# Kernel optimization log

Hardware: AMD Instinct MI355X
Metric: run time of the kernel (lower is better)

## Reference

```python
import jax, jax.numpy as jnp
import numpy as np

B, N, DIM = 4, 2048, 1024
HEADS, DHEAD = 16, 64
INNER = HEADS * DHEAD  # 1024


def _sigma(t):
    # elu(x) + 1 feature map (strictly positive)
    return jax.nn.elu(t) + 1.0


def setup_inputs() -> dict:
    key = jax.random.key(0)
    k1, k2, k3, k4, k5 = jax.random.split(key, 5)
    x = jax.random.normal(k1, (B, N, DIM), dtype=jnp.float32)
    M = jax.random.normal(k2, (B, HEADS, DHEAD, DHEAD), dtype=jnp.float32)
    Z = jnp.ones((B, HEADS, DHEAD, 1), dtype=jnp.float32)
    W_qkv = jax.random.normal(k3, (DIM, 3 * INNER), dtype=jnp.float32) * (DIM ** -0.5)
    beta_lin = jnp.ones((1,), dtype=jnp.float32) * 4.6     # Linear_Attention.beta
    beta_gate = jax.random.normal(k4, (1, HEADS, 1, 1), dtype=jnp.float32)  # per-head gate
    return {"x": x, "M": M, "Z": Z, "W_qkv": W_qkv, "beta_lin": beta_lin, "beta_gate": beta_gate}


def reference(x, M, Z, W_qkv, beta_lin, beta_gate):
    b, n, _ = x.shape
    scale = DHEAD ** -0.5

    qkv = x @ W_qkv                                   # [b, n, 3*inner]
    q, k, v = jnp.split(qkv, 3, axis=-1)
    # b n (h d) -> b h n d
    to_heads = lambda t: t.reshape(b, n, HEADS, DHEAD).transpose(0, 2, 1, 3)
    q, k, v = to_heads(q), to_heads(k), to_heads(v)

    # ---- linear-attention compressive memory branch ----
    sq = _sigma(q)                                    # [b h n d]
    sk = _sigma(k)
    A_mem = jnp.einsum('bhnd,bhdv->bhnv', sq, M) / jnp.einsum('bhnd,bhdi->bhni', sq, Z)
    moment = jnp.einsum('bhnd,bhdv->bhnv', sk, M) / jnp.einsum('bhnd,bhdi->bhni', sk, Z)

    # EMA state update (training path)
    beta_m = jnp.clip(jax.nn.sigmoid(beta_lin), 0.9, 0.999)  # scalar in (0.9, 0.999)
    Z_new = beta_m * Z + jnp.sum(sk, axis=-2)[..., None]      # [b h d 1]
    M_new = beta_m * M + jnp.einsum('bhnd,bhnv->bhdv', sk, v - moment)

    # ---- standard dot-product attention branch ----
    dots = jnp.einsum('bhid,bhjd->bhij', q, k) * scale
    attn = jax.nn.softmax(dots, axis=-1)
    A_dot = jnp.einsum('bhij,bhjd->bhid', attn, v)

    # ---- learned per-head gate ----
    g = jax.nn.sigmoid(beta_gate)                     # [1 h 1 1]
    A = g * A_mem + (1.0 - g) * A_dot                 # [b h n d]
    A = A.transpose(0, 2, 1, 3).reshape(b, n, INNER)  # b h n d -> b n (h d)
    return (A, M_new, Z_new)
```

## Files before the change

kernel.cpp:

```cpp
#include <hip/hip_runtime.h>
#include <math.h>

#define B_ 4
#define N_ 2048
#define DIM_ 1024
#define H_ 16
#define D_ 64
#define INNER_ 1024
#define BH_ (B_*H_)

#define A_ELEMS  (B_*N_*INNER_)
#define M_ELEMS  (BH_*D_*D_)
#define Z_ELEMS  (BH_*D_)

typedef __attribute__((ext_vector_type(8))) short short8;
typedef __attribute__((ext_vector_type(4))) float f32x4;
typedef __attribute__((ext_vector_type(4))) unsigned short us4;
typedef unsigned short u16;

__device__ __forceinline__ u16 f2bf(float f) {
    unsigned int u = __float_as_uint(f);
    u += 0x7fffu + ((u >> 16) & 1u);
    return (u16)(u >> 16);
}
__device__ __forceinline__ float bf2f(u16 s) {
    return __uint_as_float(((unsigned int)s) << 16);
}
__device__ __forceinline__ float sigma_f(float x) {
    return x > 0.f ? x + 1.f : __expf(x);
}
__device__ __forceinline__ short8 sig8(short8 in) {
    short8 out;
    u16* ip = (u16*)&in; u16* op = (u16*)&out;
    #pragma unroll
    for (int c = 0; c < 8; c++) op[c] = f2bf(sigma_f(bf2f(ip[c])));
    return out;
}

__global__ __launch_bounds__(256) void cvt_x(const float* __restrict__ x,
                                             u16* __restrict__ xb) {
    long i = ((long)blockIdx.x * 256 + threadIdx.x) * 4;
    float4 f = *(const float4*)&x[i];
    us4 o = {f2bf(f.x), f2bf(f.y), f2bf(f.z), f2bf(f.w)};
    *(us4*)&xb[i] = o;
}

__global__ __launch_bounds__(256) void cvt_w(const float* __restrict__ W,
                                             u16* __restrict__ Wt) {
    __shared__ u16 T[64 * 68];
    const int t  = threadIdx.x;
    const int n0 = blockIdx.x * 64, k0 = blockIdx.y * 64;
    #pragma unroll
    for (int i = 0; i < 4; i++) {
        int r  = (t >> 4) + i * 16;
        int c4 = (t & 15) * 4;
        float4 f = *(const float4*)&W[(long)(k0 + r) * 3072 + n0 + c4];
        T[(c4 + 0) * 68 + r] = f2bf(f.x);
        T[(c4 + 1) * 68 + r] = f2bf(f.y);
        T[(c4 + 2) * 68 + r] = f2bf(f.z);
        T[(c4 + 3) * 68 + r] = f2bf(f.w);
    }
    __syncthreads();
    #pragma unroll
    for (int i = 0; i < 4; i++) {
        int n  = (t >> 4) + i * 16;
        int k4 = (t & 15) * 4;
        us4 o;
        o.x = T[n * 68 + k4];     o.y = T[n * 68 + k4 + 1];
        o.z = T[n * 68 + k4 + 2]; o.w = T[n * 68 + k4 + 3];
        *(us4*)&Wt[(long)(n0 + n) * 1024 + k0 + k4] = o;
    }
}

__global__ __launch_bounds__(256) void qkv_mfma(
    const u16* __restrict__ xb, const u16* __restrict__ Wt,
    u16* __restrict__ q, u16* __restrict__ k, u16* __restrict__ v) {
    __shared__ u16 As[128 * 40];
    __shared__ u16 Bs[128 * 40];
    const int t = threadIdx.x, w = t >> 6, lane = t & 63;
    const int quad = lane >> 4, l16 = lane & 15;
    const int m0 = blockIdx.y * 128, j0 = blockIdx.x * 128;
    const int mw = (w >> 1) * 64, nw = (w & 1) * 64;

    f32x4 acc[4][4] = {};

    for (int k0 = 0; k0 < DIM_; k0 += 32) {
        __syncthreads();
        #pragma unroll
        for (int i = 0; i < 2; i++) {
            int r = (t >> 2) + i * 64, kg = (t & 3) * 8;
            *(short8*)&As[r * 40 + kg] =
                *(const short8*)&xb[(long)(m0 + r) * 1024 + k0 + kg];
            *(short8*)&Bs[r * 40 + kg] =
                *(const short8*)&Wt[(long)(j0 + r) * 1024 + k0 + kg];
        }
        __syncthreads();

        short8 af[4], bf[4];
        #pragma unroll
        for (int mt = 0; mt < 4; mt++)
            af[mt] = *(const short8*)&As[(mw + mt * 16 + l16) * 40 + quad * 8];
        #pragma unroll
        for (int nt = 0; nt < 4; nt++)
            bf[nt] = *(const short8*)&Bs[(nw + nt * 16 + l16) * 40 + quad * 8];
        #pragma unroll
        for (int mt = 0; mt < 4; mt++)
            #pragma unroll
            for (int nt = 0; nt < 4; nt++)
                acc[mt][nt] = __builtin_amdgcn_mfma_f32_16x16x32_bf16(
                    af[mt], bf[nt], acc[mt][nt], 0, 0, 0);
    }

    #pragma unroll
    for (int mt = 0; mt < 4; mt++) {
        #pragma unroll
        for (int r = 0; r < 4; r++) {
            int mm = m0 + mw + mt * 16 + quad * 4 + r;
            int b  = mm >> 11, n = mm & 2047;
            #pragma unroll
            for (int nt = 0; nt < 4; nt++) {
                int col   = j0 + nw + nt * 16 + l16;
                int which = col >> 10;
                int rem   = col & 1023;
                int h = rem >> 6, d = rem & 63;
                u16* dst = (which == 0) ? q : (which == 1) ? k : v;
                dst[(((long)(b * H_ + h)) * N_ + n) * D_ + d] =
                    f2bf(acc[mt][nt][r]);
            }
        }
    }
}

__global__ __launch_bounds__(256) void init_mz(
    const float* __restrict__ M, const float* __restrict__ Z,
    const float* __restrict__ beta_lin,
    float* __restrict__ outM, float* __restrict__ outZ) {
    float beta = 1.f / (1.f + __expf(-beta_lin[0]));
    beta = fminf(fmaxf(beta, 0.9f), 0.999f);
    int i = blockIdx.x * 256 + threadIdx.x;
    if (i < M_ELEMS) outM[i] = beta * M[i];
    if (i < Z_ELEMS) outZ[i] = beta * Z[i];
}

__global__ __launch_bounds__(256) void linear_mfma(
    const u16* __restrict__ qg, const u16* __restrict__ kg_,
    const u16* __restrict__ vg, const float* __restrict__ Mg,
    const float* __restrict__ Zg, const float* __restrict__ beta_gate,
    float* __restrict__ outA, float* __restrict__ outM, float* __restrict__ outZ) {
    __shared__ u16 MTz[80 * 72];
    __shared__ u16 sqsh[64 * 72];
    __shared__ u16 sksh[64 * 72];
    __shared__ u16 skT[64 * 72];
    __shared__ u16 vT[64 * 72];
    __shared__ u16 vmT[80 * 72];
    __shared__ float dks[64];

    const int bh = blockIdx.y, b = bh >> 4, h = bh & 15;
    const int t = threadIdx.x, w = t >> 6, lane = t & 63;
    const int quad = lane >> 4, l16 = lane & 15;
    const long bhN = (long)bh * N_;

    #pragma unroll
    for (int i = 0; i < 4; i++) {
        int d  = (t >> 4) + i * 16;
        int c4 = (t & 15) * 4;
        float4 f = *(const float4*)&Mg[bh * 4096 + d * 64 + c4];
        MTz[(c4 + 0) * 72 + d] = f2bf(f.x);
        MTz[(c4 + 1) * 72 + d] = f2bf(f.y);
        MTz[(c4 + 2) * 72 + d] = f2bf(f.z);
        MTz[(c4 + 3) * 72 + d] = f2bf(f.w);
    }
    if (t < 64) {
        MTz[64 * 72 + t] = f2bf(Zg[bh * 64 + t]);
        vmT[64 * 72 + t] = f2bf(1.0f);
    }
    for (int e = t; e < 15 * 72; e += 256) {
        MTz[65 * 72 + e] = 0;
        vmT[65 * 72 + e] = 0;
    }
    if (t >= 64 && t < 72) { MTz[64 * 72 + t] = 0; vmT[64 * 72 + t] = 0; }

    const float g = 1.f / (1.f + __expf(-beta_gate[h]));

    f32x4 macc[5] = {};

    const int jj = t >> 3;
    const int kgp = (t & 7) * 8;

    for (int c0 = 0; c0 < 256; c0 += 64) {
        const int n0c = blockIdx.x * 256 + c0;
        __syncthreads();

        #pragma unroll
        for (int i = 0; i < 2; i++) {
            int j = jj + i * 32;
            long gb = ((bhN + n0c + j) << 6) + kgp;
            short8 q8 = sig8(*(const short8*)&qg[gb]);
            short8 k8 = sig8(*(const short8*)&kg_[gb]);
            short8 v8 = *(const short8*)&vg[gb];
            *(short8*)&sqsh[j * 72 + kgp] = q8;
            *(short8*)&sksh[j * 72 + kgp] = k8;
            u16* kp = (u16*)&k8;
            u16* vp = (u16*)&v8;
            int jc = j ^ kgp;
            #pragma unroll
            for (int c = 0; c < 8; c++) {
                skT[(kgp + c) * 72 + jc] = kp[c];
                vT[(kgp + c) * 72 + jc]  = vp[c];
            }
        }
        __syncthreads();

        {
            short8 a0 = *(const short8*)&sqsh[(w * 16 + l16) * 72 + quad * 8];
            short8 a1 = *(const short8*)&sqsh[(w * 16 + l16) * 72 + 32 + quad * 8];
            f32x4 am[5];
            #pragma unroll
            for (int ct = 0; ct < 5; ct++) {
                short8 b0 = *(const short8*)&MTz[(ct * 16 + l16) * 72 + quad * 8];
                short8 b1 = *(const short8*)&MTz[(ct * 16 + l16) * 72 + 32 + quad * 8];
                f32x4 acc = {};
                acc = __builtin_amdgcn_mfma_f32_16x16x32_bf16(a0, b0, acc, 0, 0, 0);
                acc = __builtin_amdgcn_mfma_f32_16x16x32_bf16(a1, b1, acc, 0, 0, 0);
                am[ct] = acc;
            }
            #pragma unroll
            for (int r = 0; r < 4; r++) {
                float dq  = __shfl(am[4][r], lane & 48, 64);
                float inv = __builtin_amdgcn_rcpf(dq);
                int n = n0c + w * 16 + quad * 4 + r;
                long row = ((long)(b * N_ + n)) * INNER_ + h * 64;
                #pragma unroll
                for (int ct = 0; ct < 4; ct++)
                    outA[row + ct * 16 + l16] = g * am[ct][r] * inv;
            }
        }

        f32x4 mt_[4];
        {
            short8 a0 = *(const short8*)&MTz[(w * 16 + l16) * 72 + quad * 8];
            short8 a1 = *(const short8*)&MTz[(w * 16 + l16) * 72 + 32 + quad * 8];
            #pragma unroll
            for (int ct = 0; ct < 4; ct++) {
                short8 b0 = *(const short8*)&sksh[(ct * 16 + l16) * 72 + quad * 8];
                short8 b1 = *(const short8*)&sksh[(ct * 16 + l16) * 72 + 32 + quad * 8];
                f32x4 acc = {};
                acc = __builtin_amdgcn_mfma_f32_16x16x32_bf16(a0, b0, acc, 0, 0, 0);
                acc = __builtin_amdgcn_mfma_f32_16x16x32_bf16(a1, b1, acc, 0, 0, 0);
                mt_[ct] = acc;
            }
            short8 z0 = *(const short8*)&MTz[(64 + l16) * 72 + quad * 8];
            short8 z1 = *(const short8*)&MTz[(64 + l16) * 72 + 32 + quad * 8];
            short8 b0 = *(const short8*)&sksh[(w * 16 + l16) * 72 + quad * 8];
            short8 b1 = *(const short8*)&sksh[(w * 16 + l16) * 72 + 32 + quad * 8];
            f32x4 acc = {};
            acc = __builtin_amdgcn_mfma_f32_16x16x32_bf16(z0, b0, acc, 0, 0, 0);
            acc = __builtin_amdgcn_mfma_f32_16x16x32_bf16(z1, b1, acc, 0, 0, 0);
            if (quad == 0) dks[w * 16 + l16] = __builtin_amdgcn_rcpf(acc[0]);
        }
        __syncthreads();

        #pragma unroll
        for (int ct = 0; ct < 4; ct++) {
            float invdk = dks[ct * 16 + l16];
            #pragma unroll
            for (int r = 0; r < 4; r++) {
                int vd = w * 16 + quad * 4 + r;
                float vv = bf2f(vT[vd * 72 + ((ct * 16 + l16) ^ (vd & 56))]);
                vmT[vd * 72 + ct * 16 + l16] = f2bf(vv - mt_[ct][r] * invdk);
            }
        }
        __syncthreads();

        {
            int drow = w * 16 + l16, xr = drow & 56;
            short8 a0 = *(const short8*)&skT[drow * 72 + ((quad * 8) ^ xr)];
            short8 a1 = *(const short8*)&skT[drow * 72 + ((32 + quad * 8) ^ xr)];
            #pragma unroll
            for (int ct = 0; ct < 5; ct++) {
                short8 b0 = *(const short8*)&vmT[(ct * 16 + l16) * 72 + quad * 8];
                short8 b1 = *(const short8*)&vmT[(ct * 16 + l16) * 72 + 32 + quad * 8];
                macc[ct] = __builtin_amdgcn_mfma_f32_16x16x32_bf16(a0, b0, macc[ct], 0, 0, 0);
                macc[ct] = __builtin_amdgcn_mfma_f32_16x16x32_bf16(a1, b1, macc[ct], 0, 0, 0);
            }
        }
    }

    #pragma unroll
    for (int ct = 0; ct < 4; ct++)
        #pragma unroll
        for (int r = 0; r < 4; r++) {
            int d = w * 16 + quad * 4 + r;
            atomicAdd(&outM[bh * 4096 + d * 64 + ct * 16 + l16], macc[ct][r]);
        }
    if (l16 == 0)
        #pragma unroll
        for (int r = 0; r < 4; r++)
            atomicAdd(&outZ[bh * 64 + w * 16 + quad * 4 + r], macc[4][r]);
}

__global__ __launch_bounds__(256) void flash_mfma(
    const u16* __restrict__ qb, const u16* __restrict__ kb,
    const u16* __restrict__ vb, const float* __restrict__ beta_gate,
    float* __restrict__ outA) {
    __shared__ u16 Ks[64 * 72];
    __shared__ u16 Vt[64 * 72];
    __shared__ u16 Ps[4][32 * 72];

    const int bh = blockIdx.y, b = bh >> 4, h = bh & 15;
    const int n0 = blockIdx.x * 128;
    const int t = threadIdx.x, w = t >> 6, lane = t & 63;
    const int quad = lane >> 4, l16 = lane & 15;
    const long bhN = (long)bh * N_;

    short8 qf[2][2];
    #pragma unroll
    for (int mi = 0; mi < 2; mi++) {
        long qrow = bhN + n0 + w * 32 + mi * 16 + l16;
        qf[mi][0] = *(const short8*)&qb[(qrow << 6) + quad * 8];
        qf[mi][1] = *(const short8*)&qb[(qrow << 6) + 32 + quad * 8];
    }

    f32x4 of[2][4] = {};
    float lpart[2] = {0.f, 0.f};

    for (int j0 = 0; j0 < N_; j0 += 64) {
        __syncthreads();
        #pragma unroll
        for (int i = 0; i < 2; i++) {
            int j  = (t >> 3) + i * 32;
            int kg = (t & 7) * 8;
            long gbase = ((bhN + j0 + j) << 6) + kg;
            *(short8*)&Ks[j * 72 + kg] = *(const short8*)&kb[gbase];
            short8 vv = *(const short8*)&vb[gbase];
            u16* vp = (u16*)&vv;
            int jc = j ^ kg;
            #pragma unroll
            for (int c = 0; c < 8; c++) Vt[(kg + c) * 72 + jc] = vp[c];
        }
        __syncthreads();

        #pragma unroll
        for (int kt = 0; kt < 4; kt++) {
            short8 kf0 = *(const short8*)&Ks[(kt * 16 + l16) * 72 + quad * 8];
            short8 kf1 = *(const short8*)&Ks[(kt * 16 + l16) * 72 + 32 + quad * 8];
            #pragma unroll
            for (int mi = 0; mi < 2; mi++) {
                f32x4 st = {};
                st = __builtin_amdgcn_mfma_f32_16x16x32_bf16(kf0, qf[mi][0], st, 0, 0, 0);
                st = __builtin_amdgcn_mfma_f32_16x16x32_bf16(kf1, qf[mi][1], st, 0, 0, 0);
                float p0 = __expf(st[0] * 0.125f);
                float p1 = __expf(st[1] * 0.125f);
                float p2 = __expf(st[2] * 0.125f);
                float p3 = __expf(st[3] * 0.125f);
                lpart[mi] += (p0 + p1) + (p2 + p3);
                uint2 pk;
                pk.x = (__float_as_uint(p0) >> 16) | (__float_as_uint(p1) & 0xFFFF0000u);
                pk.y = (__float_as_uint(p2) >> 16) | (__float_as_uint(p3) & 0xFFFF0000u);
                *(uint2*)&Ps[w][(mi * 16 + l16) * 72 + kt * 16 + quad * 4] = pk;
            }
        }

        #pragma unroll
        for (int s = 0; s < 2; s++) {
            short8 af0 = *(const short8*)&Ps[w][(l16) * 72 + s * 32 + quad * 8];
            short8 af1 = *(const short8*)&Ps[w][(16 + l16) * 72 + s * 32 + quad * 8];
            #pragma unroll
            for (int nt = 0; nt < 4; nt++) {
                int d  = nt * 16 + l16;
                int xr = d & 56;
                short8 vf = *(const short8*)&Vt[d * 72 + ((s * 32 + quad * 8) ^ xr)];
                of[0][nt] = __builtin_amdgcn_mfma_f32_16x16x32_bf16(af0, vf, of[0][nt], 0, 0, 0);
                of[1][nt] = __builtin_amdgcn_mfma_f32_16x16x32_bf16(af1, vf, of[1][nt], 0, 0, 0);
            }
        }
    }

    const float g  = 1.f / (1.f + __expf(-beta_gate[h]));
    const float gi = 1.f - g;
    #pragma unroll
    for (int mi = 0; mi < 2; mi++) {
        float lr = lpart[mi];
        lr += __shfl_xor(lr, 16, 64);
        lr += __shfl_xor(lr, 32, 64);
        float linv = 1.f / lr;
        #pragma unroll
        for (int r = 0; r < 4; r++) {
            float lv = __shfl(linv, quad * 4 + r, 64);
            int n = n0 + w * 32 + mi * 16 + quad * 4 + r;
            #pragma unroll
            for (int nt = 0; nt < 4; nt++) {
                long idx = ((long)(b * N_ + n)) * INNER_ + h * 64 + nt * 16 + l16;
                outA[idx] += gi * of[mi][nt][r] * lv;
            }
        }
    }
}

extern "C" void kernel_launch(void* const* d_in, const int* in_sizes, int n_in,
                              void* d_out, int out_size, void* d_ws, size_t ws_size,
                              hipStream_t stream) {
    const float* x         = (const float*)d_in[0];
    const float* M         = (const float*)d_in[1];
    const float* Z         = (const float*)d_in[2];
    const float* W         = (const float*)d_in[3];
    const float* beta_lin  = (const float*)d_in[4];
    const float* beta_gate = (const float*)d_in[5];

    float* out  = (float*)d_out;
    float* outA = out;
    float* outM = out + A_ELEMS;
    float* outZ = out + A_ELEMS + M_ELEMS;

    u16* xb = (u16*)d_ws;
    u16* Wt = xb + (size_t)8192 * 1024;
    u16* qb = Wt + (size_t)3072 * 1024;
    u16* kb = qb + (size_t)BH_ * N_ * D_;
    u16* vb = kb + (size_t)BH_ * N_ * D_;

    cvt_x<<<dim3(A_ELEMS / 1024), 256, 0, stream>>>(x, xb);
    cvt_w<<<dim3(48, 16), 256, 0, stream>>>(W, Wt);
    qkv_mfma<<<dim3(24, 64), 256, 0, stream>>>(xb, Wt, qb, kb, vb);
    init_mz<<<dim3((M_ELEMS + 255) / 256), 256, 0, stream>>>(M, Z, beta_lin, outM, outZ);
    linear_mfma<<<dim3(8, BH_), 256, 0, stream>>>(qb, kb, vb, M, Z, beta_gate,
                                                  outA, outM, outZ);
    flash_mfma<<<dim3(N_ / 128, BH_), 256, 0, stream>>>(qb, kb, vb, beta_gate, outA);
}
```

Before: 309.5 us.

## Store V pre-transposed from QKV GEMM and register-prefetch K/V tiles in flash kernel

The QKV GEMM epilogue now writes V in a [bh, d, n] transposed layout, so the linear and flash kernels can stage V into shared memory with vector stores instead of scalar transposing scatters. The flash kernel also prefetches the next K/V tile into registers while the current tile is being computed. It additionally replaces expf with exp2 using a prescaled constant and uses a byte-permute to pack bf16 values. The transposed V writes in the GEMM epilogue are strided scalar stores, which may cost more, and the prefetch increases register pressure.

```diff
diff --git a/kernel.cpp b/kernel.cpp
--- a/kernel.cpp
+++ b/kernel.cpp
@@ -12,6 +12,8 @@
 #define A_ELEMS  (B_*N_*INNER_)
 #define M_ELEMS  (BH_*D_*D_)
 #define Z_ELEMS  (BH_*D_)
+
+#define SC_LOG2E 0.18033688011112042f
 
 typedef __attribute__((ext_vector_type(8))) short short8;
 typedef __attribute__((ext_vector_type(4))) float f32x4;
@@ -74,7 +76,7 @@
 
 __global__ __launch_bounds__(256) void qkv_mfma(
     const u16* __restrict__ xb, const u16* __restrict__ Wt,
-    u16* __restrict__ q, u16* __restrict__ k, u16* __restrict__ v) {
+    u16* __restrict__ q, u16* __restrict__ k, u16* __restrict__ vT) {
     __shared__ u16 As[128 * 40];
     __shared__ u16 Bs[128 * 40];
     const int t = threadIdx.x, w = t >> 6, lane = t & 63;
@@ -123,9 +125,13 @@
                 int which = col >> 10;
                 int rem   = col & 1023;
                 int h = rem >> 6, d = rem & 63;
-                u16* dst = (which == 0) ? q : (which == 1) ? k : v;
-                dst[(((long)(b * H_ + h)) * N_ + n) * D_ + d] =
-                    f2bf(acc[mt][nt][r]);
+                u16 val = f2bf(acc[mt][nt][r]);
+                if (which == 2) {
+                    vT[((long)(b * H_ + h) * 64 + d) * 2048 + n] = val;
+                } else {
+                    u16* dst = (which == 0) ? q : k;
+                    dst[(((long)(b * H_ + h)) * N_ + n) * D_ + d] = val;
+                }
             }
         }
     }
@@ -144,7 +150,7 @@
 
 __global__ __launch_bounds__(256) void linear_mfma(
     const u16* __restrict__ qg, const u16* __restrict__ kg_,
-    const u16* __restrict__ vg, const float* __restrict__ Mg,
+    const u16* __restrict__ vTg, const float* __restrict__ Mg,
     const float* __restrict__ Zg, const float* __restrict__ beta_gate,
     float* __restrict__ outA, float* __restrict__ outM, float* __restrict__ outZ) {
     __shared__ u16 MTz[80 * 72];
@@ -186,6 +192,8 @@
 
     const int jj = t >> 3;
     const int kgp = (t & 7) * 8;
+    const int srow = t >> 2;
+    const int sg   = (t & 3) * 16;
 
     for (int c0 = 0; c0 < 256; c0 += 64) {
         const int n0c = blockIdx.x * 256 + c0;
@@ -197,17 +205,17 @@
             long gb = ((bhN + n0c + j) << 6) + kgp;
             short8 q8 = sig8(*(const short8*)&qg[gb]);
             short8 k8 = sig8(*(const short8*)&kg_[gb]);
-            short8 v8 = *(const short8*)&vg[gb];
             *(short8*)&sqsh[j * 72 + kgp] = q8;
             *(short8*)&sksh[j * 72 + kgp] = k8;
             u16* kp = (u16*)&k8;
-            u16* vp = (u16*)&v8;
             int jc = j ^ kgp;
             #pragma unroll
-            for (int c = 0; c < 8; c++) {
-                skT[(kgp + c) * 72 + jc] = kp[c];
-                vT[(kgp + c) * 72 + jc]  = vp[c];
-            }
+            for (int c = 0; c < 8; c++) skT[(kgp + c) * 72 + jc] = kp[c];
+        }
+        {
+            const u16* vp = vTg + ((long)bh * 64 + srow) * 2048 + n0c + sg;
+            *(short8*)&vT[srow * 72 + sg]     = *(const short8*)vp;
+            *(short8*)&vT[srow * 72 + sg + 8] = *(const short8*)(vp + 8);
         }
         __syncthreads();
 
@@ -266,7 +274,7 @@
             #pragma unroll
             for (int r = 0; r < 4; r++) {
                 int vd = w * 16 + quad * 4 + r;
-                float vv = bf2f(vT[vd * 72 + ((ct * 16 + l16) ^ (vd & 56))]);
+                float vv = bf2f(vT[vd * 72 + ct * 16 + l16]);
                 vmT[vd * 72 + ct * 16 + l16] = f2bf(vv - mt_[ct][r] * invdk);
             }
         }
@@ -301,7 +309,7 @@
 
 __global__ __launch_bounds__(256) void flash_mfma(
     const u16* __restrict__ qb, const u16* __restrict__ kb,
-    const u16* __restrict__ vb, const float* __restrict__ beta_gate,
+    const u16* __restrict__ vTg, const float* __restrict__ beta_gate,
     float* __restrict__ outA) {
     __shared__ u16 Ks[64 * 72];
     __shared__ u16 Vt[64 * 72];
@@ -313,6 +321,11 @@
     const int quad = lane >> 4, l16 = lane & 15;
     const long bhN = (long)bh * N_;
 
+    const int srow = t >> 2;
+    const int sg   = (t & 3) * 16;
+    const u16* kbase  = kb + (bhN << 6);
+    const u16* vtbase = vTg + (long)bh * 64 * 2048;
+
     short8 qf[2][2];
     #pragma unroll
     for (int mi = 0; mi < 2; mi++) {
@@ -321,24 +334,35 @@
         qf[mi][1] = *(const short8*)&qb[(qrow << 6) + 32 + quad * 8];
     }
 
+    short8 kr0, kr1, vr0, vr1;
+    {
+        const u16* kp = kbase + ((long)srow << 6) + sg;
+        kr0 = *(const short8*)kp;
+        kr1 = *(const short8*)(kp + 8);
+        const u16* vp = vtbase + (long)srow * 2048 + sg;
+        vr0 = *(const short8*)vp;
+        vr1 = *(const short8*)(vp + 8);
+    }
+
     f32x4 of[2][4] = {};
     float lpart[2] = {0.f, 0.f};
 
     for (int j0 = 0; j0 < N_; j0 += 64) {
         __syncthreads();
-        #pragma unroll
-        for (int i = 0; i < 2; i++) {
-            int j  = (t >> 3) + i * 32;
-            int kg = (t & 7) * 8;
-            long gbase = ((bhN + j0 + j) << 6) + kg;
-            *(short8*)&Ks[j * 72 + kg] = *(const short8*)&kb[gbase];
-            short8 vv = *(const short8*)&vb[gbase];
-            u16* vp = (u16*)&vv;
-            int jc = j ^ kg;
-            #pragma unroll
-            for (int c = 0; c < 8; c++) Vt[(kg + c) * 72 + jc] = vp[c];
-        }
-        __syncthreads();
+        *(short8*)&Ks[srow * 72 + sg]     = kr0;
+        *(short8*)&Ks[srow * 72 + sg + 8] = kr1;
+        *(short8*)&Vt[srow * 72 + sg]     = vr0;
+        *(short8*)&Vt[srow * 72 + sg + 8] = vr1;
+        __syncthreads();
+
+        if (j0 + 64 < N_) {
+            const u16* kp = kbase + ((long)(j0 + 64 + srow) << 6) + sg;
+            kr0 = *(const short8*)kp;
+            kr1 = *(const short8*)(kp + 8);
+            const u16* vp = vtbase + (long)srow * 2048 + j0 + 64 + sg;
+            vr0 = *(const short8*)vp;
+            vr1 = *(const short8*)(vp + 8);
+        }
 
         #pragma unroll
         for (int kt = 0; kt < 4; kt++) {
@@ -349,14 +373,16 @@
                 f32x4 st = {};
                 st = __builtin_amdgcn_mfma_f32_16x16x32_bf16(kf0, qf[mi][0], st, 0, 0, 0);
                 st = __builtin_amdgcn_mfma_f32_16x16x32_bf16(kf1, qf[mi][1], st, 0, 0, 0);
-                float p0 = __expf(st[0] * 0.125f);
-                float p1 = __expf(st[1] * 0.125f);
-                float p2 = __expf(st[2] * 0.125f);
-                float p3 = __expf(st[3] * 0.125f);
+                float p0 = __builtin_amdgcn_exp2f(st[0] * SC_LOG2E);
+                float p1 = __builtin_amdgcn_exp2f(st[1] * SC_LOG2E);
+                float p2 = __builtin_amdgcn_exp2f(st[2] * SC_LOG2E);
+                float p3 = __builtin_amdgcn_exp2f(st[3] * SC_LOG2E);
                 lpart[mi] += (p0 + p1) + (p2 + p3);
                 uint2 pk;
-                pk.x = (__float_as_uint(p0) >> 16) | (__float_as_uint(p1) & 0xFFFF0000u);
-                pk.y = (__float_as_uint(p2) >> 16) | (__float_as_uint(p3) & 0xFFFF0000u);
+                pk.x = __builtin_amdgcn_perm(__float_as_uint(p1), __float_as_uint(p0),
+                                             0x07060302u);
+                pk.y = __builtin_amdgcn_perm(__float_as_uint(p3), __float_as_uint(p2),
+                                             0x07060302u);
                 *(uint2*)&Ps[w][(mi * 16 + l16) * 72 + kt * 16 + quad * 4] = pk;
             }
         }
@@ -367,9 +393,7 @@
             short8 af1 = *(const short8*)&Ps[w][(16 + l16) * 72 + s * 32 + quad * 8];
             #pragma unroll
             for (int nt = 0; nt < 4; nt++) {
-                int d  = nt * 16 + l16;
-                int xr = d & 56;
-                short8 vf = *(const short8*)&Vt[d * 72 + ((s * 32 + quad * 8) ^ xr)];
+                short8 vf = *(const short8*)&Vt[(nt * 16 + l16) * 72 + s * 32 + quad * 8];
                 of[0][nt] = __builtin_amdgcn_mfma_f32_16x16x32_bf16(af0, vf, of[0][nt], 0, 0, 0);
                 of[1][nt] = __builtin_amdgcn_mfma_f32_16x16x32_bf16(af1, vf, of[1][nt], 0, 0, 0);
             }
@@ -416,13 +440,13 @@
     u16* Wt = xb + (size_t)8192 * 1024;
     u16* qb = Wt + (size_t)3072 * 1024;
     u16* kb = qb + (size_t)BH_ * N_ * D_;
-    u16* vb = kb + (size_t)BH_ * N_ * D_;
+    u16* vt = kb + (size_t)BH_ * N_ * D_;
 
     cvt_x<<<dim3(A_ELEMS / 1024), 256, 0, stream>>>(x, xb);
     cvt_w<<<dim3(48, 16), 256, 0, stream>>>(W, Wt);
-    qkv_mfma<<<dim3(24, 64), 256, 0, stream>>>(xb, Wt, qb, kb, vb);
+    qkv_mfma<<<dim3(24, 64), 256, 0, stream>>>(xb, Wt, qb, kb, vt);
     init_mz<<<dim3((M_ELEMS + 255) / 256), 256, 0, stream>>>(M, Z, beta_lin, outM, outZ);
-    linear_mfma<<<dim3(8, BH_), 256, 0, stream>>>(qb, kb, vb, M, Z, beta_gate,
+    linear_mfma<<<dim3(8, BH_), 256, 0, stream>>>(qb, kb, vt, M, Z, beta_gate,
                                                   outA, outM, outZ);
-    flash_mfma<<<dim3(N_ / 128, BH_), 256, 0, stream>>>(qb, kb, vb, beta_gate, outA);
-}
+    flash_mfma<<<dim3(N_ / 128, BH_), 256, 0, stream>>>(qb, kb, vt, beta_gate, outA);
+}
```

After: 324.5 us. 1.05x slower.

## Pre-transpose V and split flash attention keys across waves, reading K/V from global

Applied to the files above, without the earlier changes.

A new kernel writes V transposed to workspace once, so the linear and flash kernels no longer transpose V through LDS on every tile. The flash kernel now gives each block 64 query rows and splits the key range across its four waves. Each wave loads K and V^T fragments straight from global memory into registers, with no LDS staging or per-tile barriers. The P fragments are built in registers with byte permutes and exp2, and the per-wave partial outputs are reduced through LDS at the end. This removes the per-iteration LDS traffic and syncs, at the cost of an extra transpose pass, more global/L2 reads, higher register pressure, and twice as many flash blocks.

```diff
diff --git a/kernel.cpp b/kernel.cpp
--- a/kernel.cpp
+++ b/kernel.cpp
@@ -12,6 +12,8 @@
 #define A_ELEMS  (B_*N_*INNER_)
 #define M_ELEMS  (BH_*D_*D_)
 #define Z_ELEMS  (BH_*D_)
+
+#define SC_LOG2E 0.18033688011112042f
 
 typedef __attribute__((ext_vector_type(8))) short short8;
 typedef __attribute__((ext_vector_type(4))) float f32x4;
@@ -131,6 +133,31 @@
     }
 }
 
+__global__ __launch_bounds__(256) void vt_transpose(
+    const u16* __restrict__ vb, u16* __restrict__ vT) {
+    __shared__ u16 T[64 * 72];
+    const int bh = blockIdx.y;
+    const int n0 = blockIdx.x * 64;
+    const int t  = threadIdx.x;
+    const int jj = t >> 3, kg = (t & 7) * 8;
+    #pragma unroll
+    for (int i = 0; i < 2; i++) {
+        int j = jj + i * 32;
+        short8 vv = *(const short8*)&vb[(((long)bh * N_ + n0 + j) << 6) + kg];
+        u16* vp = (u16*)&vv;
+        int jc = j ^ kg;
+        #pragma unroll
+        for (int c = 0; c < 8; c++) T[(kg + c) * 72 + jc] = vp[c];
+    }
+    __syncthreads();
+    const int d = t >> 2, sg = (t & 3) * 16, xr = d & 56;
+    short8 a0 = *(const short8*)&T[d * 72 + (sg ^ xr)];
+    short8 a1 = *(const short8*)&T[d * 72 + ((sg + 8) ^ xr)];
+    u16* dst = vT + ((long)bh * 64 + d) * 2048 + n0 + sg;
+    *(short8*)dst       = a0;
+    *(short8*)(dst + 8) = a1;
+}
+
 __global__ __launch_bounds__(256) void init_mz(
     const float* __restrict__ M, const float* __restrict__ Z,
     const float* __restrict__ beta_lin,
@@ -144,7 +171,7 @@
 
 __global__ __launch_bounds__(256) void linear_mfma(
     const u16* __restrict__ qg, const u16* __restrict__ kg_,
-    const u16* __restrict__ vg, const float* __restrict__ Mg,
+    const u16* __restrict__ vTg, const float* __restrict__ Mg,
     const float* __restrict__ Zg, const float* __restrict__ beta_gate,
     float* __restrict__ outA, float* __restrict__ outM, float* __restrict__ outZ) {
     __shared__ u16 MTz[80 * 72];
@@ -186,6 +213,8 @@
 
     const int jj = t >> 3;
     const int kgp = (t & 7) * 8;
+    const int srow = t >> 2;
+    const int sg   = (t & 3) * 16;
 
     for (int c0 = 0; c0 < 256; c0 += 64) {
         const int n0c = blockIdx.x * 256 + c0;
@@ -197,17 +226,17 @@
             long gb = ((bhN + n0c + j) << 6) + kgp;
             short8 q8 = sig8(*(const short8*)&qg[gb]);
             short8 k8 = sig8(*(const short8*)&kg_[gb]);
-            short8 v8 = *(const short8*)&vg[gb];
             *(short8*)&sqsh[j * 72 + kgp] = q8;
             *(short8*)&sksh[j * 72 + kgp] = k8;
             u16* kp = (u16*)&k8;
-            u16* vp = (u16*)&v8;
             int jc = j ^ kgp;
             #pragma unroll
-            for (int c = 0; c < 8; c++) {
-                skT[(kgp + c) * 72 + jc] = kp[c];
-                vT[(kgp + c) * 72 + jc]  = vp[c];
-            }
+            for (int c = 0; c < 8; c++) skT[(kgp + c) * 72 + jc] = kp[c];
+        }
+        {
+            const u16* vp = vTg + ((long)bh * 64 + srow) * 2048 + n0c + sg;
+            *(short8*)&vT[srow * 72 + sg]     = *(const short8*)vp;
+            *(short8*)&vT[srow * 72 + sg + 8] = *(const short8*)(vp + 8);
         }
         __syncthreads();
 
@@ -266,7 +295,7 @@
             #pragma unroll
             for (int r = 0; r < 4; r++) {
                 int vd = w * 16 + quad * 4 + r;
-                float vv = bf2f(vT[vd * 72 + ((ct * 16 + l16) ^ (vd & 56))]);
+                float vv = bf2f(vT[vd * 72 + ct * 16 + l16]);
                 vmT[vd * 72 + ct * 16 + l16] = f2bf(vv - mt_[ct][r] * invdk);
             }
         }
@@ -301,99 +330,121 @@
 
 __global__ __launch_bounds__(256) void flash_mfma(
     const u16* __restrict__ qb, const u16* __restrict__ kb,
-    const u16* __restrict__ vb, const float* __restrict__ beta_gate,
+    const u16* __restrict__ vTg, const float* __restrict__ beta_gate,
     float* __restrict__ outA) {
-    __shared__ u16 Ks[64 * 72];
-    __shared__ u16 Vt[64 * 72];
-    __shared__ u16 Ps[4][32 * 72];
+    __shared__ float Osh[64 * 65];
+    __shared__ float lsh[64];
 
     const int bh = blockIdx.y, b = bh >> 4, h = bh & 15;
-    const int n0 = blockIdx.x * 128;
+    const int n0 = blockIdx.x * 64;
     const int t = threadIdx.x, w = t >> 6, lane = t & 63;
     const int quad = lane >> 4, l16 = lane & 15;
     const long bhN = (long)bh * N_;
 
-    short8 qf[2][2];
-    #pragma unroll
-    for (int mi = 0; mi < 2; mi++) {
-        long qrow = bhN + n0 + w * 32 + mi * 16 + l16;
+    short8 qf[4][2];
+    #pragma unroll
+    for (int mi = 0; mi < 4; mi++) {
+        long qrow = bhN + n0 + mi * 16 + l16;
         qf[mi][0] = *(const short8*)&qb[(qrow << 6) + quad * 8];
         qf[mi][1] = *(const short8*)&qb[(qrow << 6) + 32 + quad * 8];
     }
 
-    f32x4 of[2][4] = {};
-    float lpart[2] = {0.f, 0.f};
-
-    for (int j0 = 0; j0 < N_; j0 += 64) {
-        __syncthreads();
-        #pragma unroll
-        for (int i = 0; i < 2; i++) {
-            int j  = (t >> 3) + i * 32;
-            int kg = (t & 7) * 8;
-            long gbase = ((bhN + j0 + j) << 6) + kg;
-            *(short8*)&Ks[j * 72 + kg] = *(const short8*)&kb[gbase];
-            short8 vv = *(const short8*)&vb[gbase];
-            u16* vp = (u16*)&vv;
-            int jc = j ^ kg;
-            #pragma unroll
-            for (int c = 0; c < 8; c++) Vt[(kg + c) * 72 + jc] = vp[c];
-        }
-        __syncthreads();
-
-        #pragma unroll
-        for (int kt = 0; kt < 4; kt++) {
-            short8 kf0 = *(const short8*)&Ks[(kt * 16 + l16) * 72 + quad * 8];
-            short8 kf1 = *(const short8*)&Ks[(kt * 16 + l16) * 72 + 32 + quad * 8];
-            #pragma unroll
-            for (int mi = 0; mi < 2; mi++) {
-                f32x4 st = {};
-                st = __builtin_amdgcn_mfma_f32_16x16x32_bf16(kf0, qf[mi][0], st, 0, 0, 0);
-                st = __builtin_amdgcn_mfma_f32_16x16x32_bf16(kf1, qf[mi][1], st, 0, 0, 0);
-                float p0 = __expf(st[0] * 0.125f);
-                float p1 = __expf(st[1] * 0.125f);
-                float p2 = __expf(st[2] * 0.125f);
-                float p3 = __expf(st[3] * 0.125f);
-                lpart[mi] += (p0 + p1) + (p2 + p3);
-                uint2 pk;
-                pk.x = (__float_as_uint(p0) >> 16) | (__float_as_uint(p1) & 0xFFFF0000u);
-                pk.y = (__float_as_uint(p2) >> 16) | (__float_as_uint(p3) & 0xFFFF0000u);
-                *(uint2*)&Ps[w][(mi * 16 + l16) * 72 + kt * 16 + quad * 4] = pk;
-            }
-        }
-
-        #pragma unroll
-        for (int s = 0; s < 2; s++) {
-            short8 af0 = *(const short8*)&Ps[w][(l16) * 72 + s * 32 + quad * 8];
-            short8 af1 = *(const short8*)&Ps[w][(16 + l16) * 72 + s * 32 + quad * 8];
-            #pragma unroll
-            for (int nt = 0; nt < 4; nt++) {
-                int d  = nt * 16 + l16;
-                int xr = d & 56;
-                short8 vf = *(const short8*)&Vt[d * 72 + ((s * 32 + quad * 8) ^ xr)];
-                of[0][nt] = __builtin_amdgcn_mfma_f32_16x16x32_bf16(af0, vf, of[0][nt], 0, 0, 0);
-                of[1][nt] = __builtin_amdgcn_mfma_f32_16x16x32_bf16(af1, vf, of[1][nt], 0, 0, 0);
-            }
-        }
+    const u16* kbase  = kb + (bhN << 6);
+    const u16* vtbase = vTg + (long)bh * 64 * 2048;
+    const int  kperm  = (l16 >> 2) * 8 + (l16 & 3);
+
+    f32x4 of[4][4] = {};
+    float lpart[4] = {0.f, 0.f, 0.f, 0.f};
+
+    for (int it = 0; it < 16; it++) {
+        const int kb0 = w * 512 + it * 32;
+
+        const u16* kp0 = kbase + ((long)(kb0 + kperm) << 6) + quad * 8;
+        const u16* kp1 = kp0 + (4 << 6);
+        short8 kf0a = *(const short8*)kp0;
+        short8 kf0b = *(const short8*)(kp0 + 32);
+        short8 kf1a = *(const short8*)kp1;
+        short8 kf1b = *(const short8*)(kp1 + 32);
+
+        short8 vf[4];
+        #pragma unroll
+        for (int nt = 0; nt < 4; nt++)
+            vf[nt] = *(const short8*)&vtbase[((long)(nt * 16 + l16)) * 2048
+                                             + kb0 + quad * 8];
+
+        #pragma unroll
+        for (int mi = 0; mi < 4; mi++) {
+            f32x4 st0 = {}, st1 = {};
+            st0 = __builtin_amdgcn_mfma_f32_16x16x32_bf16(kf0a, qf[mi][0], st0, 0, 0, 0);
+            st0 = __builtin_amdgcn_mfma_f32_16x16x32_bf16(kf0b, qf[mi][1], st0, 0, 0, 0);
+            st1 = __builtin_amdgcn_mfma_f32_16x16x32_bf16(kf1a, qf[mi][0], st1, 0, 0, 0);
+            st1 = __builtin_amdgcn_mfma_f32_16x16x32_bf16(kf1b, qf[mi][1], st1, 0, 0, 0);
+            float p0 = __builtin_amdgcn_exp2f(st0[0] * SC_LOG2E);
+            float p1 = __builtin_amdgcn_exp2f(st0[1] * SC_LOG2E);
+            float p2 = __builtin_amdgcn_exp2f(st0[2] * SC_LOG2E);
+            float p3 = __builtin_amdgcn_exp2f(st0[3] * SC_LOG2E);
+            float p4 = __builtin_amdgcn_exp2f(st1[0] * SC_LOG2E);
+            float p5 = __builtin_amdgcn_exp2f(st1[1] * SC_LOG2E);
+            float p6 = __builtin_amdgcn_exp2f(st1[2] * SC_LOG2E);
+            float p7 = __builtin_amdgcn_exp2f(st1[3] * SC_LOG2E);
+            lpart[mi] += ((p0 + p1) + (p2 + p3)) + ((p4 + p5) + (p6 + p7));
+            short8 af;
+            unsigned int* au = (unsigned int*)&af;
+            au[0] = __builtin_amdgcn_perm(__float_as_uint(p1), __float_as_uint(p0),
+                                          0x07060302u);
+            au[1] = __builtin_amdgcn_perm(__float_as_uint(p3), __float_as_uint(p2),
+                                          0x07060302u);
+            au[2] = __builtin_amdgcn_perm(__float_as_uint(p5), __float_as_uint(p4),
+                                          0x07060302u);
+            au[3] = __builtin_amdgcn_perm(__float_as_uint(p7), __float_as_uint(p6),
+                                          0x07060302u);
+            #pragma unroll
+            for (int nt = 0; nt < 4; nt++)
+                of[mi][nt] = __builtin_amdgcn_mfma_f32_16x16x32_bf16(
+                    af, vf[nt], of[mi][nt], 0, 0, 0);
+        }
+    }
+
+    #pragma unroll
+    for (int mi = 0; mi < 4; mi++) {
+        lpart[mi] += __shfl_xor(lpart[mi], 16, 64);
+        lpart[mi] += __shfl_xor(lpart[mi], 32, 64);
+    }
+    for (int ww = 0; ww < 4; ww++) {
+        if (w == ww) {
+            #pragma unroll
+            for (int mi = 0; mi < 4; mi++) {
+                if (quad == 0) {
+                    if (ww == 0) lsh[mi * 16 + l16] = lpart[mi];
+                    else         lsh[mi * 16 + l16] += lpart[mi];
+                }
+                #pragma unroll
+                for (int nt = 0; nt < 4; nt++)
+                    #pragma unroll
+                    for (int r = 0; r < 4; r++) {
+                        int row = mi * 16 + quad * 4 + r;
+                        int col = nt * 16 + l16;
+                        if (ww == 0) Osh[row * 65 + col] = of[mi][nt][r];
+                        else         Osh[row * 65 + col] += of[mi][nt][r];
+                    }
+            }
+        }
+        __syncthreads();
     }
 
     const float g  = 1.f / (1.f + __expf(-beta_gate[h]));
     const float gi = 1.f - g;
-    #pragma unroll
-    for (int mi = 0; mi < 2; mi++) {
-        float lr = lpart[mi];
-        lr += __shfl_xor(lr, 16, 64);
-        lr += __shfl_xor(lr, 32, 64);
-        float linv = 1.f / lr;
-        #pragma unroll
-        for (int r = 0; r < 4; r++) {
-            float lv = __shfl(linv, quad * 4 + r, 64);
-            int n = n0 + w * 32 + mi * 16 + quad * 4 + r;
-            #pragma unroll
-            for (int nt = 0; nt < 4; nt++) {
-                long idx = ((long)(b * N_ + n)) * INNER_ + h * 64 + nt * 16 + l16;
-                outA[idx] += gi * of[mi][nt][r] * lv;
-            }
-        }
+    const int row  = w * 16 + l16;
+    const float sc = gi / lsh[row];
+    float* orow = outA + ((long)(b * N_ + n0 + row)) * INNER_ + h * 64;
+    #pragma unroll
+    for (int i = 0; i < 4; i++) {
+        int d0 = quad * 4 + i * 16;
+        float4 o4 = *(float4*)&Osh[row * 65 + d0];
+        float4 a4 = *(float4*)&orow[d0];
+        a4.x += sc * o4.x; a4.y += sc * o4.y;
+        a4.z += sc * o4.z; a4.w += sc * o4.w;
+        *(float4*)&orow[d0] = a4;
     }
 }
 
@@ -417,12 +468,14 @@
     u16* qb = Wt + (size_t)3072 * 1024;
     u16* kb = qb + (size_t)BH_ * N_ * D_;
     u16* vb = kb + (size_t)BH_ * N_ * D_;
+    u16* vt = vb + (size_t)BH_ * N_ * D_;
 
     cvt_x<<<dim3(A_ELEMS / 1024), 256, 0, stream>>>(x, xb);
     cvt_w<<<dim3(48, 16), 256, 0, stream>>>(W, Wt);
     qkv_mfma<<<dim3(24, 64), 256, 0, stream>>>(xb, Wt, qb, kb, vb);
+    vt_transpose<<<dim3(N_ / 64, BH_), 256, 0, stream>>>(vb, vt);
     init_mz<<<dim3((M_ELEMS + 255) / 256), 256, 0, stream>>>(M, Z, beta_lin, outM, outZ);
-    linear_mfma<<<dim3(8, BH_), 256, 0, stream>>>(qb, kb, vb, M, Z, beta_gate,
+    linear_mfma<<<dim3(8, BH_), 256, 0, stream>>>(qb, kb, vt, M, Z, beta_gate,
                                                   outA, outM, outZ);
-    flash_mfma<<<dim3(N_ / 128, BH_), 256, 0, stream>>>(qb, kb, vb, beta_gate, outA);
-}
+    flash_mfma<<<dim3(N_ / 64, BH_), 256, 0, stream>>>(qb, kb, vt, beta_gate, outA);
+}
```

Measured after the change: 346.6 us. +12.0%, slower.
